# Kernel optimization log

Hardware: AMD Instinct MI355X
Metric: run time of the kernel (lower is better)

The kernel has to match this reference:

```python
import jax, jax.numpy as jnp
import numpy as np

E = 256      # embed_dim
TD = 128     # token_dim
NH = 8       # num_heads
HD = E // NH
FF = 4 * E
EPS = 1e-5


def ln(x, g, b):
    m = jnp.mean(x, axis=-1, keepdims=True)
    v = jnp.mean((x - m) ** 2, axis=-1, keepdims=True)
    return (x - m) * jax.lax.rsqrt(v + EPS) * g + b


def setup_inputs() -> dict:
    key = jax.random.key(0)
    ks = jax.random.split(key, 20)
    B, H, W = 16, 64, 64
    s = lambda d: 1.0 / np.sqrt(d)
    inp = {
        "image_embeddings": jax.random.normal(ks[0], (B, E, H, W), jnp.float32),
        "target_token": jax.random.normal(ks[1], (B, TD), jnp.float32),
        "bg_token": jax.random.normal(ks[2], (B, TD), jnp.float32),
        # token_proj
        "Wp": jax.random.normal(ks[3], (E, TD), jnp.float32) * s(TD),
        "bp": jnp.zeros((E,), jnp.float32),
        # layernorms
        "g_img": jnp.ones((E,), jnp.float32), "b_img": jnp.zeros((E,), jnp.float32),
        "g_tok": jnp.ones((E,), jnp.float32), "b_tok": jnp.zeros((E,), jnp.float32),
        "g_ffn": jnp.ones((E,), jnp.float32), "b_ffn": jnp.zeros((E,), jnp.float32),
        # attention projections (in_proj split into q/k/v)
        "Wq": jax.random.normal(ks[4], (E, E), jnp.float32) * s(E),
        "Wk": jax.random.normal(ks[5], (E, E), jnp.float32) * s(E),
        "Wv": jax.random.normal(ks[6], (E, E), jnp.float32) * s(E),
        "bq": jnp.zeros((E,), jnp.float32),
        "bk": jnp.zeros((E,), jnp.float32),
        "bv": jnp.zeros((E,), jnp.float32),
        "Wo": jax.random.normal(ks[7], (E, E), jnp.float32) * s(E),
        "bo": jnp.zeros((E,), jnp.float32),
        # ffn
        "W1": jax.random.normal(ks[8], (FF, E), jnp.float32) * s(E),
        "b1": jnp.zeros((FF,), jnp.float32),
        "W2": jax.random.normal(ks[9], (E, FF), jnp.float32) * s(FF),
        "b2": jnp.zeros((E,), jnp.float32),
    }
    return inp


def reference(image_embeddings, target_token, bg_token, Wp, bp,
              g_img, b_img, g_tok, b_tok, g_ffn, b_ffn,
              Wq, Wk, Wv, bq, bk, bv, Wo, bo, W1, b1, W2, b2):
    B, C, H, W = image_embeddings.shape
    # tokens -> embed space, stacked as KV of length 2
    tgt = target_token @ Wp.T + bp          # [B,E]
    bg = bg_token @ Wp.T + bp               # [B,E]
    token_kv = jnp.stack([tgt, bg], axis=1)  # [B,2,E]

    x = image_embeddings.reshape(B, C, H * W).transpose(0, 2, 1)  # [B,N,E]

    # pre-norm cross attention (dropout=0 at inference)
    qn = ln(x, g_img, b_img)
    kvn = ln(token_kv, g_tok, b_tok)
    q = (qn @ Wq.T + bq).reshape(B, -1, NH, HD)   # [B,N,h,d]
    k = (kvn @ Wk.T + bk).reshape(B, 2, NH, HD)    # [B,2,h,d]
    v = (kvn @ Wv.T + bv).reshape(B, 2, NH, HD)
    scores = jnp.einsum('bnhd,bkhd->bhnk', q, k) / np.sqrt(HD)  # [B,h,N,2]
    attn = jax.nn.softmax(scores, axis=-1)
    ctx = jnp.einsum('bhnk,bkhd->bnhd', attn, v).reshape(B, -1, E)
    attended = ctx @ Wo.T + bo

    x = x + attended
    h = jax.nn.gelu(ln(x, g_ffn, b_ffn) @ W1.T + b1, approximate=False)
    x = x + (h @ W2.T + b2)
    return x.transpose(0, 2, 1).reshape(B, C, H, W)
```

## Files before the change

kernel.cpp:

```cpp
#include <hip/hip_runtime.h>
#include <math.h>

#define E 256
#define TD 128
#define FF 1024
#define NTOK 4096

typedef __attribute__((ext_vector_type(8))) __bf16 bf16x8;
typedef __attribute__((ext_vector_type(4))) float f32x4;

__device__ __forceinline__ unsigned short f2bf(float x) {
    __bf16 b = (__bf16)x;
    return __builtin_bit_cast(unsigned short, b);
}
__device__ __forceinline__ float bf2f(unsigned short h) {
    return __uint_as_float(((unsigned)h) << 16);
}
__device__ __forceinline__ float gelu_fast(float x) {
    float ex = __expf(-x * (1.5957691216057308f + 0.07135481627f * x * x));
    return x * __builtin_amdgcn_rcpf(1.f + ex);
}
__device__ __forceinline__ void bar_lds() {
    __builtin_amdgcn_sched_barrier(0);
    asm volatile("s_waitcnt lgkmcnt(0)" ::: "memory");
    __builtin_amdgcn_s_barrier();
    __builtin_amdgcn_sched_barrier(0);
}
__device__ __forceinline__ void gll16(const unsigned short* g, unsigned short* l) {
    __builtin_amdgcn_global_load_lds(
        (const __attribute__((address_space(1))) unsigned int*)g,
        (__attribute__((address_space(3))) unsigned int*)l, 16, 0, 0);
}

#define WVM1 asm volatile("s_waitcnt vmcnt(1)" ::: "memory")
#define WVM0 asm volatile("s_waitcnt vmcnt(0)" ::: "memory")
#define WAITV(S) do { if ((S) <= 126) { WVM1; } else { WVM0; } } while (0)

__global__ __launch_bounds__(256) void prep_kernel(
    const float* __restrict__ W1, const float* __restrict__ W2, const float* __restrict__ b1,
    const float* __restrict__ tt, const float* __restrict__ bgt,
    const float* __restrict__ Wp, const float* __restrict__ bp,
    const float* __restrict__ g_tok, const float* __restrict__ b_tok,
    const float* __restrict__ g_img, const float* __restrict__ b_img,
    const float* __restrict__ Wq, const float* __restrict__ bq,
    const float* __restrict__ Wk, const float* __restrict__ bk,
    const float* __restrict__ Wv, const float* __restrict__ bv,
    const float* __restrict__ Wo,
    const float* __restrict__ g_ffn, const float* __restrict__ b_ffn,
    unsigned short* __restrict__ w1s, unsigned short* __restrict__ w2s,
    unsigned short* __restrict__ wks, unsigned short* __restrict__ wvs,
    float* __restrict__ Gk, float* __restrict__ sbk,
    float* __restrict__ G1, float* __restrict__ B1)
{
    const int t = threadIdx.x;
    const int lane = t & 63;
    if (blockIdx.x < 256) {
        int gid = blockIdx.x * 256 + t;
        if (gid < 32768) {
            int row = gid >> 5;
            int k0 = (gid & 31) * 8;
            f32x4 wa = *(const f32x4*)(W1 + row * 256 + k0);
            f32x4 wb = *(const f32x4*)(W1 + row * 256 + k0 + 4);
            f32x4 ga = *(const f32x4*)(g_ffn + k0);
            f32x4 gb = *(const f32x4*)(g_ffn + k0 + 4);
            ushort4 o0, o1;
            o0.x = f2bf(wa[0]*ga[0]); o0.y = f2bf(wa[1]*ga[1]);
            o0.z = f2bf(wa[2]*ga[2]); o0.w = f2bf(wa[3]*ga[3]);
            o1.x = f2bf(wb[0]*gb[0]); o1.y = f2bf(wb[1]*gb[1]);
            o1.z = f2bf(wb[2]*gb[2]); o1.w = f2bf(wb[3]*gb[3]);
            int dst = ((row >> 4) * 8 + (k0 >> 5)) * 512 + (((k0 >> 3) & 3) * 16 + (row & 15)) * 8;
            *(ushort4*)(w1s + dst) = o0;
            *(ushort4*)(w1s + dst + 4) = o1;
        } else {
            int g2 = gid - 32768;
            int o = g2 >> 7;
            int f0 = (g2 & 127) * 8;
            f32x4 wa = *(const f32x4*)(W2 + o * 1024 + f0);
            f32x4 wb = *(const f32x4*)(W2 + o * 1024 + f0 + 4);
            ushort4 o0, o1;
            o0.x = f2bf(wa[0]); o0.y = f2bf(wa[1]); o0.z = f2bf(wa[2]); o0.w = f2bf(wa[3]);
            o1.x = f2bf(wb[0]); o1.y = f2bf(wb[1]); o1.z = f2bf(wb[2]); o1.w = f2bf(wb[3]);
            int dst = (((f0 >> 8) * 16 + (o >> 4)) * 8 + ((f0 >> 5) & 7)) * 512
                    + (((f0 >> 3) & 3) * 16 + (o & 15)) * 8;
            *(ushort4*)(w2s + dst) = o0;
            *(ushort4*)(w2s + dst + 4) = o1;
        }
        if (gid < 1024) {
            int row = gid;
            float gacc = 0.f, bacc = 0.f;
            for (int k = 0; k < 256; k += 4) {
                f32x4 w = *(const f32x4*)(W1 + row * 256 + k);
                f32x4 g = *(const f32x4*)(g_ffn + k);
                f32x4 bb = *(const f32x4*)(b_ffn + k);
                gacc += w[0]*g[0] + w[1]*g[1] + w[2]*g[2] + w[3]*g[3];
                bacc += w[0]*bb[0] + w[1]*bb[1] + w[2]*bb[2] + w[3]*bb[3];
            }
            G1[row] = gacc;
            B1[row] = bacc + b1[row];
        }
        return;
    }
    const int bi = blockIdx.x - 256;
    __shared__ float tokL[2][TD];
    __shared__ float kvn[2][E];
    __shared__ float ks[2][E];
    __shared__ float vs[2][E];
    __shared__ float red[8];
    __shared__ float redk[16][4], redb[16][4];

    if (t < TD) tokL[0][t] = tt[bi * TD + t];
    else tokL[1][t - TD] = bgt[bi * TD + (t - TD)];
    __syncthreads();

    {
        float a0 = bp[t], a1 = a0;
        const float* wr = Wp + (size_t)t * TD;
        for (int i = 0; i < TD; i += 4) {
            f32x4 w = *(const f32x4*)(wr + i);
            f32x4 x0 = *(const f32x4*)(&tokL[0][i]);
            f32x4 x1 = *(const f32x4*)(&tokL[1][i]);
            a0 += w[0]*x0[0] + w[1]*x0[1] + w[2]*x0[2] + w[3]*x0[3];
            a1 += w[0]*x1[0] + w[1]*x1[1] + w[2]*x1[2] + w[3]*x1[3];
        }
        kvn[0][t] = a0; kvn[1][t] = a1;
    }
    __syncthreads();
    for (int j = 0; j < 2; ++j) {
        float v = kvn[j][t];
        float s = v, s2 = v * v;
        for (int off = 32; off; off >>= 1) { s += __shfl_down(s, off); s2 += __shfl_down(s2, off); }
        if (lane == 0) { red[t >> 6] = s; red[4 + (t >> 6)] = s2; }
        __syncthreads();
        float S = red[0] + red[1] + red[2] + red[3];
        float S2 = red[4] + red[5] + red[6] + red[7];
        float m = S * (1.f / E);
        float rs = rsqrtf(S2 * (1.f / E) - m * m + 1e-5f);
        __syncthreads();
        kvn[j][t] = (v - m) * rs * g_tok[t] + b_tok[t];
    }
    __syncthreads();
    {
        float k0 = bk[t], k1 = k0, v0 = bv[t], v1 = v0;
        const float* wkr = Wk + (size_t)t * E;
        const float* wvr = Wv + (size_t)t * E;
        for (int i = 0; i < E; i += 4) {
            f32x4 wk4 = *(const f32x4*)(wkr + i);
            f32x4 wv4 = *(const f32x4*)(wvr + i);
            f32x4 x0 = *(const f32x4*)(&kvn[0][i]);
            f32x4 x1 = *(const f32x4*)(&kvn[1][i]);
            k0 += wk4[0]*x0[0] + wk4[1]*x0[1] + wk4[2]*x0[2] + wk4[3]*x0[3];
            k1 += wk4[0]*x1[0] + wk4[1]*x1[1] + wk4[2]*x1[2] + wk4[3]*x1[3];
            v0 += wv4[0]*x0[0] + wv4[1]*x0[1] + wv4[2]*x0[2] + wv4[3]*x0[3];
            v1 += wv4[0]*x1[0] + wv4[1]*x1[1] + wv4[2]*x1[2] + wv4[3]*x1[3];
        }
        ks[0][t] = k0; ks[1][t] = k1; vs[0][t] = v0; vs[1][t] = v1;
    }
    __syncthreads();
    const float inv = 0.17677669529663687f;
    const float gi = g_img[t], bimg = b_img[t];
    for (int c = 0; c < 16; ++c) {
        int j = c >> 3, h = c & 7;
        float awk = 0.f, awv = 0.f;
        const float* wqc = Wq + (size_t)(h * 32) * E + t;
        const float* wor = Wo + (size_t)t * E + h * 32;
        #pragma unroll
        for (int d = 0; d < 32; d += 4) {
            f32x4 kv = *(const f32x4*)(&ks[j][h * 32 + d]);
            f32x4 vv = *(const f32x4*)(&vs[j][h * 32 + d]);
            f32x4 wo4 = *(const f32x4*)(wor + d);
            awk += kv[0]*wqc[(size_t)(d+0)*E] + kv[1]*wqc[(size_t)(d+1)*E]
                 + kv[2]*wqc[(size_t)(d+2)*E] + kv[3]*wqc[(size_t)(d+3)*E];
            awv += wo4[0]*vv[0] + wo4[1]*vv[1] + wo4[2]*vv[2] + wo4[3]*vv[3];
        }
        float base = awk * inv;
        wks[(bi * 8 + (t >> 5)) * 512 + (((t >> 3) & 3) * 16 + c) * 8 + (t & 7)] = f2bf(gi * base);
        wvs[(bi * 16 + (t >> 4)) * 512 + ((c >> 3) * 16 + (t & 15)) * 8 + (c & 7)] = f2bf(awv);
        float rk = gi * base, rb = bimg * base;
        for (int off = 32; off; off >>= 1) { rk += __shfl_down(rk, off); rb += __shfl_down(rb, off); }
        if (lane == 0) { redk[c][t >> 6] = rk; redb[c][t >> 6] = rb; }
    }
    #pragma unroll
    for (int c2 = 16; c2 < 32; ++c2)
        wvs[(bi * 16 + (t >> 4)) * 512 + ((c2 >> 3) * 16 + (t & 15)) * 8 + (c2 & 7)] = 0;
    __syncthreads();
    if (t < 16) {
        int c = t, j = c >> 3, h = c & 7;
        float s = 0.f;
        for (int d = 0; d < 32; ++d) s += bq[h * 32 + d] * ks[j][h * 32 + d];
        Gk[bi * 16 + c] = redk[c][0] + redk[c][1] + redk[c][2] + redk[c][3];
        sbk[bi * 16 + c] = redb[c][0] + redb[c][1] + redb[c][2] + redb[c][3] + s * inv;
    }
}

__global__ __launch_bounds__(512, 4) void fused_main_kernel(
    const float* __restrict__ img,
    const float* __restrict__ pbo, const float* __restrict__ pb2,
    const unsigned short* __restrict__ w1s, const unsigned short* __restrict__ w2s,
    const unsigned short* __restrict__ wks, const unsigned short* __restrict__ wvs,
    const float* __restrict__ Gk, const float* __restrict__ sbk,
    const float* __restrict__ G1, const float* __restrict__ B1,
    float* __restrict__ out)
{
    __shared__ __align__(16) char smem[74240];
    unsigned short* xsf = (unsigned short*)smem;
    unsigned short* hsf = (unsigned short*)(smem + 32768);
    float* part_s  = (float*)(smem + 32768);
    float* part_s2 = (float*)(smem + 35072);
    unsigned short* alf = (unsigned short*)(smem + 32768);
    float* scf     = (float*)(smem + 37376);
    float* outsf   = (float*)(smem + 32768);
    float* mean_s  = (float*)(smem + 73728);
    float* rstd_s  = (float*)(smem + 73984);

    const int t = threadIdx.x;
    const int lane = t & 63;
    const int wid = t >> 6;
    const int l15 = lane & 15;
    const int l4 = lane >> 4;
    const int bi = blockIdx.x >> 6;
    const int n0 = (blockIdx.x & 63) << 6;
    const int nc = wid * 32;
    unsigned short* wrg = (unsigned short*)(smem + 49152) + wid * 1536;

    {
        const float* imgb = img + ((size_t)bi * E) * NTOK + n0 + lane;
        float ps = 0.f, ps2 = 0.f;
        #pragma unroll
        for (int i = 0; i < 4; ++i) {
            int e0 = wid * 8 + i * 64;
            unsigned pk[4];
            #pragma unroll
            for (int jp = 0; jp < 4; ++jp) {
                float va = __builtin_nontemporal_load(&imgb[(size_t)(e0 + 2 * jp) * NTOK]);
                float vb = __builtin_nontemporal_load(&imgb[(size_t)(e0 + 2 * jp + 1) * NTOK]);
                unsigned short ha = f2bf(va), hb = f2bf(vb);
                float fa = bf2f(ha), fb = bf2f(hb);
                ps += fa + fb; ps2 += fa * fa + fb * fb;
                pk[jp] = (unsigned)ha | ((unsigned)hb << 16);
            }
            int idx = (lane * 256 + e0) ^ ((lane & 31) << 3);
            uint4 u = {pk[0], pk[1], pk[2], pk[3]};
            *(uint4*)&xsf[idx] = u;
        }
        part_s[lane * 9 + wid] = ps;
        part_s2[lane * 9 + wid] = ps2;
    }
    __syncthreads();

    if (t < 64) {
        float s = 0.f, s2 = 0.f;
        #pragma unroll
        for (int w = 0; w < 8; ++w) { s += part_s[t * 9 + w]; s2 += part_s2[t * 9 + w]; }
        float m = s * (1.f / 256.f);
        mean_s[t] = m;
        rstd_s[t] = rsqrtf(s2 * (1.f / 256.f) - m * m + 1e-5f);
    }

    {
        const int mt = wid >> 1, kh = wid & 1;
        f32x4 p = {0.f, 0.f, 0.f, 0.f};
        #pragma unroll
        for (int kq = 0; kq < 4; ++kq) {
            int kk = kh * 4 + kq;
            int row = mt * 16 + l15;
            bf16x8 a = *(const bf16x8*)&xsf[(row * 256 + kk * 32 + l4 * 8) ^ ((row & 31) << 3)];
            bf16x8 bfr = *(const bf16x8*)&wks[(bi * 8 + kk) * 512 + lane * 8];
            p = __builtin_amdgcn_mfma_f32_16x16x32_bf16(a, bfr, p, 0, 0, 0);
        }
        #pragma unroll
        for (int rg = 0; rg < 4; ++rg)
            scf[(kh * 64 + mt * 16 + l4 * 4 + rg) * 16 + l15] = p[rg];
    }
    __syncthreads();

    {
        int r = t >> 3, h = t & 7;
        float gk0 = Gk[bi * 16 + h], gk1 = Gk[bi * 16 + 8 + h];
        float sb0 = sbk[bi * 16 + h], sb1 = sbk[bi * 16 + 8 + h];
        float ms = mean_s[r], rs = rstd_s[r];
        float raw0 = scf[r * 16 + h] + scf[(64 + r) * 16 + h];
        float raw1 = scf[r * 16 + 8 + h] + scf[(64 + r) * 16 + 8 + h];
        float s0 = rs * (raw0 - ms * gk0) + sb0;
        float s1 = rs * (raw1 - ms * gk1) + sb1;
        float mx = fmaxf(s0, s1);
        float e0 = __expf(s0 - mx), e1 = __expf(s1 - mx);
        float is = __builtin_amdgcn_rcpf(e0 + e1);
        alf[r * 32 + h] = f2bf(e0 * is);
        alf[r * 32 + 8 + h] = f2bf(e1 * is);
        alf[r * 32 + 16 + h] = 0;
        alf[r * 32 + 24 + h] = 0;
    }
    __syncthreads();

    f32x4 acc2[4][2];
    {
        f32x4 pa[4][2];
        #pragma unroll
        for (int m = 0; m < 4; ++m)
            #pragma unroll
            for (int n = 0; n < 2; ++n)
                pa[m][n] = f32x4{0.f, 0.f, 0.f, 0.f};
        bf16x8 bv[2];
        #pragma unroll
        for (int n = 0; n < 2; ++n)
            bv[n] = *(const bf16x8*)&wvs[(bi * 16 + wid * 2 + n) * 512 + lane * 8];
        #pragma unroll
        for (int m = 0; m < 4; ++m) {
            bf16x8 af = *(const bf16x8*)&alf[(m * 16 + l15) * 32 + l4 * 8];
            #pragma unroll
            for (int n = 0; n < 2; ++n)
                pa[m][n] = __builtin_amdgcn_mfma_f32_16x16x32_bf16(af, bv[n], pa[m][n], 0, 0, 0);
        }
        float bov[2], b2v[2];
        #pragma unroll
        for (int n = 0; n < 2; ++n) {
            bov[n] = pbo[nc + n * 16 + l15];
            b2v[n] = pb2[nc + n * 16 + l15];
        }
        #pragma unroll
        for (int m = 0; m < 4; ++m)
            #pragma unroll
            for (int n = 0; n < 2; ++n)
                #pragma unroll
                for (int rg = 0; rg < 4; ++rg) {
                    int R = m * 16 + l4 * 4 + rg;
                    int C = nc + n * 16 + l15;
                    int xi = (R * 256 + C) ^ ((R & 31) << 3);
                    float x1 = bf2f(xsf[xi]) + pa[m][n][rg] + bov[n];
                    xsf[xi] = f2bf(x1);
                    acc2[m][n][rg] = x1 + b2v[n];
                }
    }

    float g1pre[8], b1pre[8];
    #pragma unroll
    for (int c = 0; c < 8; ++c) {
        g1pre[c] = G1[c * 128 + wid * 16 + l15];
        b1pre[c] = B1[c * 128 + wid * 16 + l15];
    }
    __syncthreads();

    for (int rr = 0; rr < 8; ++rr) {
        int r = wid * 8 + rr;
        int idx = (r * 256 + lane * 4) ^ ((r & 31) << 3);
        ushort4 xv = *(const ushort4*)&xsf[idx];
        float v0 = bf2f(xv.x), v1 = bf2f(xv.y), v2 = bf2f(xv.z), v3 = bf2f(xv.w);
        float s = v0 + v1 + v2 + v3;
        float s2 = v0 * v0 + v1 * v1 + v2 * v2 + v3 * v3;
        for (int off = 32; off; off >>= 1) { s += __shfl_down(s, off); s2 += __shfl_down(s2, off); }
        if (lane == 0) {
            float m = s * (1.f / 256.f);
            mean_s[r] = m;
            rstd_s[r] = rsqrtf(s2 * (1.f / 256.f) - m * m + 1e-5f);
        }
    }
    __syncthreads();

    #define ISSUE(S) do { if ((S) <= 127) { \
        const int c_ = (S) >> 4, j_ = (S) & 15; \
        const unsigned short* src_; \
        if (j_ < 8) src_ = w1s + (size_t)((c_ * 64 + j_) * 512) + wid * 4096 + lane * 8; \
        else { const int kkl_ = (j_ - 8) >> 1, og_ = (j_ - 8) & 1; \
               src_ = w2s + (size_t)((((c_ >> 1) * 128 + og_ * 8 + (c_ & 1) * 4 + kkl_)) * 512) + wid * 8192 + lane * 8; } \
        gll16(src_, wrg + ((S) % 3) * 512); \
    } } while (0)

    #define G1STEP(S) { \
        WAITV(S); \
        bf16x8 bf_ = *(const bf16x8*)&wrg[((S) % 3) * 512 + lane * 8]; \
        const int kb_ = ((S) & 15) * 32 + l4 * 8; \
        bf16x8 x0_ = *(const bf16x8*)&xsf[((l15) * 256 + kb_) ^ (((l15) & 31) << 3)]; \
        bf16x8 x1_ = *(const bf16x8*)&xsf[((16 + l15) * 256 + kb_) ^ (((16 + l15) & 31) << 3)]; \
        bf16x8 x2_ = *(const bf16x8*)&xsf[((32 + l15) * 256 + kb_) ^ (((32 + l15) & 31) << 3)]; \
        bf16x8 x3_ = *(const bf16x8*)&xsf[((48 + l15) * 256 + kb_) ^ (((48 + l15) & 31) << 3)]; \
        p[0] = __builtin_amdgcn_mfma_f32_16x16x32_bf16(x0_, bf_, p[0], 0, 0, 0); \
        p[1] = __builtin_amdgcn_mfma_f32_16x16x32_bf16(x1_, bf_, p[1], 0, 0, 0); \
        p[2] = __builtin_amdgcn_mfma_f32_16x16x32_bf16(x2_, bf_, p[2], 0, 0, 0); \
        p[3] = __builtin_amdgcn_mfma_f32_16x16x32_bf16(x3_, bf_, p[3], 0, 0, 0); \
        ISSUE((S) + 2); \
    }

    #define G2STEP(S) { \
        WAITV(S); \
        bf16x8 bf_ = *(const bf16x8*)&wrg[((S) % 3) * 512 + lane * 8]; \
        if ((((S) & 15) & 1) == 0) { \
            const int cb_ = (((((S) & 15) - 8) >> 1)) * 32 + l4 * 8; \
            af2[0] = *(const bf16x8*)&hsf[((l15) * 128 + cb_) ^ ((l15) << 3)]; \
            af2[1] = *(const bf16x8*)&hsf[((16 + l15) * 128 + cb_) ^ ((l15) << 3)]; \
            af2[2] = *(const bf16x8*)&hsf[((32 + l15) * 128 + cb_) ^ ((l15) << 3)]; \
            af2[3] = *(const bf16x8*)&hsf[((48 + l15) * 128 + cb_) ^ ((l15) << 3)]; \
        } \
        { const int og_ = ((S) & 15) & 1; \
          acc2[0][og_] = __builtin_amdgcn_mfma_f32_16x16x32_bf16(af2[0], bf_, acc2[0][og_], 0, 0, 0); \
          acc2[1][og_] = __builtin_amdgcn_mfma_f32_16x16x32_bf16(af2[1], bf_, acc2[1][og_], 0, 0, 0); \
          acc2[2][og_] = __builtin_amdgcn_mfma_f32_16x16x32_bf16(af2[2], bf_, acc2[2][og_], 0, 0, 0); \
          acc2[3][og_] = __builtin_amdgcn_mfma_f32_16x16x32_bf16(af2[3], bf_, acc2[3][og_], 0, 0, 0); } \
        ISSUE((S) + 2); \
    }

    #define GELUC(C) { \
        const float g1v_ = g1pre[(C)], b1v_ = b1pre[(C)]; \
        _Pragma("unroll") \
        for (int m_ = 0; m_ < 4; ++m_) { \
            _Pragma("unroll") \
            for (int rg_ = 0; rg_ < 4; ++rg_) { \
                int R_ = m_ * 16 + l4 * 4 + rg_; \
                float hp_ = rstd_s[R_] * (p[m_][rg_] - mean_s[R_] * g1v_) + b1v_; \
                hsf[(R_ * 128 + wid * 16 + l15) ^ ((R_ & 15) << 3)] = f2bf(gelu_fast(hp_)); \
            } \
            p[m_] = f32x4{0.f, 0.f, 0.f, 0.f}; \
        } \
    }

    #define CHUNK(C) { \
        G1STEP((C)*16 + 0); G1STEP((C)*16 + 1); G1STEP((C)*16 + 2); G1STEP((C)*16 + 3); \
        G1STEP((C)*16 + 4); G1STEP((C)*16 + 5); G1STEP((C)*16 + 6); G1STEP((C)*16 + 7); \
        GELUC(C); \
        bar_lds(); \
        G2STEP((C)*16 + 8);  G2STEP((C)*16 + 9);  G2STEP((C)*16 + 10); G2STEP((C)*16 + 11); \
        G2STEP((C)*16 + 12); G2STEP((C)*16 + 13); G2STEP((C)*16 + 14); G2STEP((C)*16 + 15); \
        bar_lds(); \
    }

    f32x4 p[4];
    #pragma unroll
    for (int m = 0; m < 4; ++m) p[m] = f32x4{0.f, 0.f, 0.f, 0.f};
    bf16x8 af2[4];

    ISSUE(0); ISSUE(1);
    CHUNK(0) CHUNK(1) CHUNK(2) CHUNK(3) CHUNK(4) CHUNK(5) CHUNK(6) CHUNK(7)

    #undef ISSUE
    #undef G1STEP
    #undef G2STEP
    #undef GELUC
    #undef CHUNK

    #pragma unroll
    for (int h = 0; h < 2; ++h) {
        if ((wid >> 2) == h) {
            #pragma unroll
            for (int m = 0; m < 4; ++m)
                #pragma unroll
                for (int n = 0; n < 2; ++n)
                    #pragma unroll
                    for (int rg = 0; rg < 4; ++rg) {
                        int R = m * 16 + l4 * 4 + rg;
                        int Cl = nc + n * 16 + l15 - h * 128;
                        outsf[(R * 128 + Cl) ^ ((R & 7) << 2)] = acc2[m][n][rg];
                    }
        }
        __syncthreads();
        #pragma unroll
        for (int j = 0; j < 4; ++j) {
            int gidx = j * 512 + t;
            int e = gidx >> 4;
            int part = gidx & 15;
            f32x4 v;
            #pragma unroll
            for (int k2 = 0; k2 < 4; ++k2) {
                int nrow = part * 4 + k2;
                v[k2] = outsf[(nrow * 128 + e) ^ ((nrow & 7) << 2)];
            }
            __builtin_nontemporal_store(v,
                (f32x4*)(out + ((size_t)bi * E + h * 128 + e) * NTOK + n0 + part * 4));
        }
        if (h == 0) __syncthreads();
    }
}

extern "C" void kernel_launch(void* const* d_in, const int* in_sizes, int n_in,
                              void* d_out, int out_size, void* d_ws, size_t ws_size,
                              hipStream_t stream) {
    (void)in_sizes; (void)n_in; (void)out_size; (void)ws_size;
    const float* img   = (const float*)d_in[0];
    const float* tt    = (const float*)d_in[1];
    const float* bgt   = (const float*)d_in[2];
    const float* Wp    = (const float*)d_in[3];
    const float* bp    = (const float*)d_in[4];
    const float* g_img = (const float*)d_in[5];
    const float* b_img = (const float*)d_in[6];
    const float* g_tok = (const float*)d_in[7];
    const float* b_tok = (const float*)d_in[8];
    const float* g_ffn = (const float*)d_in[9];
    const float* b_ffn = (const float*)d_in[10];
    const float* Wq    = (const float*)d_in[11];
    const float* Wk    = (const float*)d_in[12];
    const float* Wv    = (const float*)d_in[13];
    const float* bq    = (const float*)d_in[14];
    const float* bk    = (const float*)d_in[15];
    const float* bv    = (const float*)d_in[16];
    const float* Wo    = (const float*)d_in[17];
    const float* bo    = (const float*)d_in[18];
    const float* W1    = (const float*)d_in[19];
    const float* b1    = (const float*)d_in[20];
    const float* W2    = (const float*)d_in[21];
    const float* b2    = (const float*)d_in[22];

    char* ws = (char*)d_ws;
    unsigned short* w1s = (unsigned short*)(ws);
    unsigned short* w2s = (unsigned short*)(ws + 524288);
    unsigned short* wks = (unsigned short*)(ws + 1048576);
    unsigned short* wvs = (unsigned short*)(ws + 1179648);
    float*          Gk  = (float*)(ws + 1441792);
    float*          sbk = (float*)(ws + 1442816);
    float*          G1  = (float*)(ws + 1443840);
    float*          B1  = (float*)(ws + 1447936);

    hipLaunchKernelGGL(prep_kernel, dim3(272), dim3(256), 0, stream,
                       W1, W2, b1, tt, bgt, Wp, bp, g_tok, b_tok, g_img, b_img,
                       Wq, bq, Wk, bk, Wv, bv, Wo, g_ffn, b_ffn,
                       w1s, w2s, wks, wvs, Gk, sbk, G1, B1);
    hipLaunchKernelGGL(fused_main_kernel, dim3(1024), dim3(512), 0, stream,
                       img, bo, b2, w1s, w2s, wks, wvs, Gk, sbk, G1, B1, (float*)d_out);
}
```

Measured before the change: 262.4 us.

## Deepen weight prefetch to 4 stages and pre-normalize x before FFN GEMMs

Weight staging goes from a 3-slot ring with prefetch distance 2 to a 4-slot ring with distance 3, waiting on vmcnt(2). The wait is moved after the LDS reads of activations so global loads have more time to land. The FFN layernorm is now applied to xsf in place before GEMM1, which removes the per-element mean/rstd/G1 correction from the GELU epilogue. LDS grows to 80KB, which may cut how many blocks fit per CU. Normalizing in bf16 before the GEMM also changes rounding slightly.

Result: faster. 241.9 us (-7.8%).

```diff
diff --git a/kernel.cpp b/kernel.cpp
--- a/kernel.cpp
+++ b/kernel.cpp
@@ -32,9 +32,10 @@
         (__attribute__((address_space(3))) unsigned int*)l, 16, 0, 0);
 }
 
+#define WVM2 asm volatile("s_waitcnt vmcnt(2)" ::: "memory")
 #define WVM1 asm volatile("s_waitcnt vmcnt(1)" ::: "memory")
 #define WVM0 asm volatile("s_waitcnt vmcnt(0)" ::: "memory")
-#define WAITV(S) do { if ((S) <= 126) { WVM1; } else { WVM0; } } while (0)
+#define WAITV(S) do { if ((S) <= 125) { WVM2; } else if ((S) == 126) { WVM1; } else { WVM0; } } while (0)
 
 __global__ __launch_bounds__(256) void prep_kernel(
     const float* __restrict__ W1, const float* __restrict__ W2, const float* __restrict__ b1,
@@ -198,19 +199,19 @@
     const unsigned short* __restrict__ w1s, const unsigned short* __restrict__ w2s,
     const unsigned short* __restrict__ wks, const unsigned short* __restrict__ wvs,
     const float* __restrict__ Gk, const float* __restrict__ sbk,
-    const float* __restrict__ G1, const float* __restrict__ B1,
+    const float* __restrict__ B1,
     float* __restrict__ out)
 {
-    __shared__ __align__(16) char smem[74240];
+    __shared__ __align__(16) char smem[81920];
     unsigned short* xsf = (unsigned short*)smem;
-    unsigned short* hsf = (unsigned short*)(smem + 32768);
+    unsigned short* hsf = (unsigned short*)(smem + 65536);
     float* part_s  = (float*)(smem + 32768);
     float* part_s2 = (float*)(smem + 35072);
     unsigned short* alf = (unsigned short*)(smem + 32768);
     float* scf     = (float*)(smem + 37376);
     float* outsf   = (float*)(smem + 32768);
-    float* mean_s  = (float*)(smem + 73728);
-    float* rstd_s  = (float*)(smem + 73984);
+    float* mean_s  = (float*)(smem + 65536);
+    float* rstd_s  = (float*)(smem + 65792);
 
     const int t = threadIdx.x;
     const int lane = t & 63;
@@ -220,7 +221,7 @@
     const int bi = blockIdx.x >> 6;
     const int n0 = (blockIdx.x & 63) << 6;
     const int nc = wid * 32;
-    unsigned short* wrg = (unsigned short*)(smem + 49152) + wid * 1536;
+    unsigned short* wrg = (unsigned short*)(smem + 32768) + wid * 2048;
 
     {
         const float* imgb = img + ((size_t)bi * E) * NTOK + n0 + lane;
@@ -332,12 +333,10 @@
                 }
     }
 
-    float g1pre[8], b1pre[8];
+    float b1pre[8];
     #pragma unroll
-    for (int c = 0; c < 8; ++c) {
-        g1pre[c] = G1[c * 128 + wid * 16 + l15];
+    for (int c = 0; c < 8; ++c)
         b1pre[c] = B1[c * 128 + wid * 16 + l15];
-    }
     __syncthreads();
 
     for (int rr = 0; rr < 8; ++rr) {
@@ -354,7 +353,7 @@
             rstd_s[r] = rsqrtf(s2 * (1.f / 256.f) - m * m + 1e-5f);
         }
     }
-    __syncthreads();
+    bar_lds();
 
     #define ISSUE(S) do { if ((S) <= 127) { \
         const int c_ = (S) >> 4, j_ = (S) & 15; \
@@ -362,27 +361,50 @@
         if (j_ < 8) src_ = w1s + (size_t)((c_ * 64 + j_) * 512) + wid * 4096 + lane * 8; \
         else { const int kkl_ = (j_ - 8) >> 1, og_ = (j_ - 8) & 1; \
                src_ = w2s + (size_t)((((c_ >> 1) * 128 + og_ * 8 + (c_ & 1) * 4 + kkl_)) * 512) + wid * 8192 + lane * 8; } \
-        gll16(src_, wrg + ((S) % 3) * 512); \
+        gll16(src_, wrg + ((S) & 3) * 512); \
     } } while (0)
 
+    ISSUE(0); ISSUE(1); ISSUE(2);
+
+    {
+        int r = t >> 3;
+        int c0 = (t & 7) * 32;
+        float mr = mean_s[r], rr2 = rstd_s[r];
+        #pragma unroll
+        for (int j = 0; j < 4; ++j) {
+            int idx = (r * 256 + c0 + j * 8) ^ ((r & 31) << 3);
+            uint4 u = *(const uint4*)&xsf[idx];
+            unsigned pk[4] = {u.x, u.y, u.z, u.w};
+            #pragma unroll
+            for (int w = 0; w < 4; ++w) {
+                float lo = bf2f((unsigned short)(pk[w] & 0xffffu));
+                float hi = bf2f((unsigned short)(pk[w] >> 16));
+                lo = (lo - mr) * rr2;
+                hi = (hi - mr) * rr2;
+                pk[w] = (unsigned)f2bf(lo) | ((unsigned)f2bf(hi) << 16);
+            }
+            uint4 o = {pk[0], pk[1], pk[2], pk[3]};
+            *(uint4*)&xsf[idx] = o;
+        }
+    }
+    bar_lds();
+
     #define G1STEP(S) { \
-        WAITV(S); \
-        bf16x8 bf_ = *(const bf16x8*)&wrg[((S) % 3) * 512 + lane * 8]; \
         const int kb_ = ((S) & 15) * 32 + l4 * 8; \
         bf16x8 x0_ = *(const bf16x8*)&xsf[((l15) * 256 + kb_) ^ (((l15) & 31) << 3)]; \
         bf16x8 x1_ = *(const bf16x8*)&xsf[((16 + l15) * 256 + kb_) ^ (((16 + l15) & 31) << 3)]; \
         bf16x8 x2_ = *(const bf16x8*)&xsf[((32 + l15) * 256 + kb_) ^ (((32 + l15) & 31) << 3)]; \
         bf16x8 x3_ = *(const bf16x8*)&xsf[((48 + l15) * 256 + kb_) ^ (((48 + l15) & 31) << 3)]; \
+        WAITV(S); \
+        bf16x8 bf_ = *(const bf16x8*)&wrg[((S) & 3) * 512 + lane * 8]; \
         p[0] = __builtin_amdgcn_mfma_f32_16x16x32_bf16(x0_, bf_, p[0], 0, 0, 0); \
         p[1] = __builtin_amdgcn_mfma_f32_16x16x32_bf16(x1_, bf_, p[1], 0, 0, 0); \
         p[2] = __builtin_amdgcn_mfma_f32_16x16x32_bf16(x2_, bf_, p[2], 0, 0, 0); \
         p[3] = __builtin_amdgcn_mfma_f32_16x16x32_bf16(x3_, bf_, p[3], 0, 0, 0); \
-        ISSUE((S) + 2); \
+        ISSUE((S) + 3); \
     }
 
     #define G2STEP(S) { \
-        WAITV(S); \
-        bf16x8 bf_ = *(const bf16x8*)&wrg[((S) % 3) * 512 + lane * 8]; \
         if ((((S) & 15) & 1) == 0) { \
             const int cb_ = (((((S) & 15) - 8) >> 1)) * 32 + l4 * 8; \
             af2[0] = *(const bf16x8*)&hsf[((l15) * 128 + cb_) ^ ((l15) << 3)]; \
@@ -390,22 +412,24 @@
             af2[2] = *(const bf16x8*)&hsf[((32 + l15) * 128 + cb_) ^ ((l15) << 3)]; \
             af2[3] = *(const bf16x8*)&hsf[((48 + l15) * 128 + cb_) ^ ((l15) << 3)]; \
         } \
+        WAITV(S); \
+        bf16x8 bf_ = *(const bf16x8*)&wrg[((S) & 3) * 512 + lane * 8]; \
         { const int og_ = ((S) & 15) & 1; \
           acc2[0][og_] = __builtin_amdgcn_mfma_f32_16x16x32_bf16(af2[0], bf_, acc2[0][og_], 0, 0, 0); \
           acc2[1][og_] = __builtin_amdgcn_mfma_f32_16x16x32_bf16(af2[1], bf_, acc2[1][og_], 0, 0, 0); \
           acc2[2][og_] = __builtin_amdgcn_mfma_f32_16x16x32_bf16(af2[2], bf_, acc2[2][og_], 0, 0, 0); \
           acc2[3][og_] = __builtin_amdgcn_mfma_f32_16x16x32_bf16(af2[3], bf_, acc2[3][og_], 0, 0, 0); } \
-        ISSUE((S) + 2); \
+        ISSUE((S) + 3); \
     }
 
     #define GELUC(C) { \
-        const float g1v_ = g1pre[(C)], b1v_ = b1pre[(C)]; \
+        const float b1v_ = b1pre[(C)]; \
         _Pragma("unroll") \
         for (int m_ = 0; m_ < 4; ++m_) { \
             _Pragma("unroll") \
             for (int rg_ = 0; rg_ < 4; ++rg_) { \
                 int R_ = m_ * 16 + l4 * 4 + rg_; \
-                float hp_ = rstd_s[R_] * (p[m_][rg_] - mean_s[R_] * g1v_) + b1v_; \
+                float hp_ = p[m_][rg_] + b1v_; \
                 hsf[(R_ * 128 + wid * 16 + l15) ^ ((R_ & 15) << 3)] = f2bf(gelu_fast(hp_)); \
             } \
             p[m_] = f32x4{0.f, 0.f, 0.f, 0.f}; \
@@ -427,7 +451,6 @@
     for (int m = 0; m < 4; ++m) p[m] = f32x4{0.f, 0.f, 0.f, 0.f};
     bf16x8 af2[4];
 
-    ISSUE(0); ISSUE(1);
     CHUNK(0) CHUNK(1) CHUNK(2) CHUNK(3) CHUNK(4) CHUNK(5) CHUNK(6) CHUNK(7)
 
     #undef ISSUE
@@ -512,5 +535,5 @@
                        Wq, bq, Wk, bk, Wv, bv, Wo, g_ffn, b_ffn,
                        w1s, w2s, wks, wvs, Gk, sbk, G1, B1);
     hipLaunchKernelGGL(fused_main_kernel, dim3(1024), dim3(512), 0, stream,
-                       img, bo, b2, w1s, w2s, wks, wvs, Gk, sbk, G1, B1, (float*)d_out);
-}
+                       img, bo, b2, w1s, w2s, wks, wvs, Gk, sbk, B1, (float*)d_out);
+}
```
